# Optimization experiments

Measured on AMD Instinct MI355X. Metric: run time of the kernel, lower is better.

Reference implementation:

```python
import jax, jax.numpy as jnp
import numpy as np

N_E, N_R, E = 100000, 1000, 1000000
E_HID, R_HID = 128, 128
NEG_SLOPE = 0.01


def _seg_softmax(logits, seg, num_segments):
    # torch_geometric.utils.softmax: per-segment max-subtracted softmax, +1e-16 in denom
    m = jax.ops.segment_max(logits, seg, num_segments=num_segments)
    m = jnp.where(jnp.isfinite(m), m, 0.0)  # empty segments
    z = jnp.exp(logits - m[seg])
    s = jax.ops.segment_sum(z, seg, num_segments=num_segments)
    return z / (s[seg] + 1e-16)


def setup_inputs() -> dict:
    key = jax.random.key(0)
    ks = jax.random.split(key, 10)
    s_e = 1.0 / np.sqrt(E_HID)
    s_r = 1.0 / np.sqrt(R_HID)
    s_2r = 1.0 / np.sqrt(2 * R_HID)
    return {
        "x_e": jax.random.normal(ks[0], (N_E, E_HID), jnp.float32),
        "x_r": jax.random.normal(ks[1], (N_R, R_HID), jnp.float32),
        "edge_index": jax.random.randint(ks[2], (2, E), 0, N_E, jnp.int32),
        "rel": jax.random.randint(ks[3], (E,), 0, N_R, jnp.int32),
        "rel_all": jax.random.randint(ks[4], (N_R,), 0, N_R, jnp.int32),
        "w_ah": jax.random.uniform(ks[5], (E_HID,), jnp.float32, -s_e, s_e),
        "w_at": jax.random.uniform(ks[6], (E_HID,), jnp.float32, -s_e, s_e),
        "w_ar": jax.random.uniform(ks[7], (R_HID,), jnp.float32, -s_r, s_r),
        "W_r1": jax.random.uniform(ks[8], (R_HID, 2 * R_HID), jnp.float32, -s_r, s_r),
        "b_r1": jnp.zeros((2 * R_HID,), jnp.float32),
        "W_r2": jax.random.uniform(ks[9], (2 * R_HID, R_HID), jnp.float32, -s_2r, s_2r),
        "b_r2": jnp.zeros((R_HID,), jnp.float32),
        "W_r": jax.random.uniform(jax.random.fold_in(key, 99), (2 * R_HID, 2 * R_HID), jnp.float32, -s_2r, s_2r),
        "b_r": jnp.zeros((2 * R_HID,), jnp.float32),
    }


def reference(x_e, x_r, edge_index, rel, rel_all, w_ah, w_at, w_ar,
              W_r1, b_r1, W_r2, b_r2, W_r, b_r):
    h, t = edge_index[0], edge_index[1]
    n_e = x_e.shape[0]

    # per-node/per-rel attention scores, gathered per edge
    e_h = (x_e @ w_ah)[h]          # [E]
    e_t = (x_e @ w_at)[t]          # [E]
    e_r = (x_r @ w_ar)[rel]        # [E]

    alpha_h = _seg_softmax(jax.nn.leaky_relu(e_h + e_r, NEG_SLOPE), h, n_e)
    alpha_t = _seg_softmax(jax.nn.leaky_relu(e_t + e_r, NEG_SLOPE), t, n_e)

    # relation transform (no activation in original)
    x_r2 = (x_r @ W_r1 + b_r1) @ W_r2 + b_r2   # [N_r, r_hidden]
    msg = x_r + x_r2                            # [N_r, r_hidden]

    # sparse.mm(adj, msg) == weighted scatter-add over edges
    msg_e = msg[rel]                            # [E, r_hidden]
    x_e_h = jax.ops.segment_sum(alpha_h[:, None] * msg_e, h, num_segments=n_e)
    x_e_t = jax.ops.segment_sum(alpha_t[:, None] * msg_e, t, num_segments=n_e)

    x = jnp.concatenate([x_e_h, x_e_t], axis=1)  # [N_e, 2*r_hidden]
    return x @ W_r + b_r
```

## Files before the change

### kernel.cpp

```cpp
#include <hip/hip_runtime.h>
#include <hip/hip_fp16.h>


#define CH1    2048
#define SUPW   4096
#define CAP1   45056
#define CH2    4096
#define CHUNK2 (CAP1 / CH2)
#define NBPS   128
#define CAP2   512
#define MAXD   64

#define MIX_LO(acc, w, z) \
    asm("v_fma_mix_f32 %0, %1, %2, %0 op_sel:[0,0,0] op_sel_hi:[1,0,0]" \
        : "+v"(acc) : "v"(w), "v"(z))
#define MIX_HI(acc, w, z) \
    asm("v_fma_mix_f32 %0, %1, %2, %0 op_sel:[1,0,0] op_sel_hi:[1,0,0]" \
        : "+v"(acc) : "v"(w), "v"(z))

__global__ __launch_bounds__(256) void k_scores(
    const float* __restrict__ xe, const float* __restrict__ xr,
    const float* __restrict__ wah, const float* __restrict__ wat, const float* __restrict__ war,
    float* __restrict__ eh, float* __restrict__ et, float* __restrict__ er,
    int nE, int nR) {
    int wid = (blockIdx.x * blockDim.x + threadIdx.x) >> 6;
    int lane = threadIdx.x & 63;
    if (wid < nE) {
        float2 x2 = *(const float2*)(xe + (size_t)wid * 128 + lane * 2);
        float2 a2 = *(const float2*)(wah + lane * 2);
        float2 b2 = *(const float2*)(wat + lane * 2);
        float dh = x2.x * a2.x + x2.y * a2.y;
        float dt = x2.x * b2.x + x2.y * b2.y;
        #pragma unroll
        for (int m = 32; m >= 1; m >>= 1) { dh += __shfl_xor(dh, m); dt += __shfl_xor(dt, m); }
        if (lane == 0) { eh[wid] = dh; et[wid] = dt; }
    } else if (wid < nE + nR) {
        int r = wid - nE;
        float2 x2 = *(const float2*)(xr + (size_t)r * 128 + lane * 2);
        float2 c2 = *(const float2*)(war + lane * 2);
        float d = x2.x * c2.x + x2.y * c2.y;
        #pragma unroll
        for (int m = 32; m >= 1; m >>= 1) d += __shfl_xor(d, m);
        if (lane == 0) er[r] = d;
    }
}

__global__ __launch_bounds__(256) void k_rel(
    const float* __restrict__ xr,
    const float* __restrict__ W1, const float* __restrict__ b1,
    const float* __restrict__ W2, const float* __restrict__ b2,
    const float* __restrict__ Wr,
    __half* __restrict__ Mh, __half* __restrict__ Mt) {
    __shared__ float xs[128];
    __shared__ float hs[256];
    __shared__ float ms[128];
    int r = blockIdx.x, j = threadIdx.x;
    if (j < 128) xs[j] = xr[(size_t)r * 128 + j];
    __syncthreads();
    {
        float acc = b1[j];
        #pragma unroll 4
        for (int k = 0; k < 128; ++k) acc += xs[k] * W1[k * 256 + j];
        hs[j] = acc;
    }
    __syncthreads();
    if (j < 128) {
        float acc = b2[j] + xs[j];
        #pragma unroll 4
        for (int k = 0; k < 256; ++k) acc += hs[k] * W2[k * 128 + j];
        ms[j] = acc;
    }
    __syncthreads();
    {
        float ah = 0.f, at_ = 0.f;
        #pragma unroll 4
        for (int i = 0; i < 128; ++i) {
            float m = ms[i];
            ah  += m * Wr[i * 256 + j];
            at_ += m * Wr[(128 + i) * 256 + j];
        }
        Mh[(size_t)r * 256 + j] = __float2half(ah);
        Mt[(size_t)r * 256 + j] = __float2half(at_);
    }
}

__global__ __launch_bounds__(256) void k_hist1(
    const int* __restrict__ ei, int* __restrict__ hist, int E) {
    __shared__ int cnt[64];
    int tid = threadIdx.x;
    if (tid < 64) cnt[tid] = 0;
    __syncthreads();
    int base = blockIdx.x * CH1;
    #pragma unroll
    for (int k = 0; k < CH1 / 256; ++k) {
        int e = base + k * 256 + tid;
        if (e < E) {
            unsigned vh = ((unsigned)ei[e]) << 1;
            unsigned vt = (((unsigned)ei[E + e]) << 1) | 1u;
            atomicAdd(&cnt[vh >> 12], 1);
            atomicAdd(&cnt[vt >> 12], 1);
        }
    }
    __syncthreads();
    if (tid < 64) hist[tid * 512 + blockIdx.x] = cnt[tid];
}

__global__ __launch_bounds__(256) void k_scanp(
    int* __restrict__ hist, int* __restrict__ bcur1,
    int* __restrict__ bcur2, int nbuck, int nblk) {
    __shared__ int wtot[4];
    int bin = blockIdx.x, tid = threadIdx.x, lane = tid & 63, wid = tid >> 6;
    for (int g = bin * 256 + tid; g < nbuck; g += 64 * 256) bcur2[g] = 0;
    int j0 = 2 * tid, j1 = 2 * tid + 1;
    int v0 = (j0 < nblk) ? hist[bin * 512 + j0] : 0;
    int v1 = (j1 < nblk) ? hist[bin * 512 + j1] : 0;
    int ts = v0 + v1;
    int incl = ts;
    #pragma unroll
    for (int d = 1; d < 64; d <<= 1) { int u = __shfl_up(incl, d); if (lane >= d) incl += u; }
    if (lane == 63) wtot[wid] = incl;
    __syncthreads();
    int wbase = 0;
    for (int w = 0; w < wid; ++w) wbase += wtot[w];
    int excl = wbase + incl - ts;
    hist[bin * 512 + j0] = excl;
    hist[bin * 512 + j1] = excl + v0;
    if (tid == 255) bcur1[bin] = wbase + incl;
}

__global__ __launch_bounds__(256) void k_part1(
    const int* __restrict__ ei, const int* __restrict__ rel,
    const int* __restrict__ hist, unsigned* __restrict__ part1, int E) {
    __shared__ unsigned stage[CH1 * 2];
    __shared__ int cnt[64], offs_[64], cur[64], gb[64];
    int tid = threadIdx.x;
    if (tid < 64) cnt[tid] = 0;
    __syncthreads();
    int base = blockIdx.x * CH1;
    unsigned wh[CH1 / 256], wt[CH1 / 256];
    bool ve[CH1 / 256];
    #pragma unroll
    for (int k = 0; k < CH1 / 256; ++k) {
        int e = base + k * 256 + tid;
        ve[k] = (e < E);
        unsigned h = 0, t = 0, r = 0;
        if (ve[k]) { h = (unsigned)ei[e]; t = (unsigned)ei[E + e]; r = (unsigned)rel[e]; }
        unsigned vh = h << 1, vt = (t << 1) | 1u;
        wh[k] = ((vh >> 12) << 26) | ((vh & 4095u) << 10) | r;
        wt[k] = ((vt >> 12) << 26) | ((vt & 4095u) << 10) | r;
        if (ve[k]) { atomicAdd(&cnt[wh[k] >> 26], 1); atomicAdd(&cnt[wt[k] >> 26], 1); }
    }
    __syncthreads();
    if (tid < 64) {
        int v = cnt[tid], incl = v;
        #pragma unroll
        for (int d = 1; d < 64; d <<= 1) { int u = __shfl_up(incl, d); if (tid >= d) incl += u; }
        offs_[tid] = incl - v;
        cur[tid] = incl - v;
        gb[tid] = hist[tid * 512 + blockIdx.x];
    }
    __syncthreads();
    #pragma unroll
    for (int k = 0; k < CH1 / 256; ++k) {
        if (ve[k]) {
            int p = atomicAdd(&cur[wh[k] >> 26], 1); stage[p] = wh[k];
            int q = atomicAdd(&cur[wt[k] >> 26], 1); stage[q] = wt[k];
        }
    }
    __syncthreads();
    int total = offs_[63] + cnt[63];
    for (int p = tid; p < total; p += 256) {
        unsigned w = stage[p];
        int bin = w >> 26;
        int dst = gb[bin] + (p - offs_[bin]);
        if (dst < CAP1) part1[(size_t)bin * CAP1 + dst] = w & 0x03FFFFFFu;
    }
}

__global__ __launch_bounds__(256) void k_part2(
    const int* __restrict__ bcur1, const unsigned* __restrict__ part1,
    int* __restrict__ bcur2, unsigned short* __restrict__ part2) {
    int s = blockIdx.x / CHUNK2, c = blockIdx.x % CHUNK2;
    int cnt_s = min(bcur1[s], CAP1);
    int start = c * CH2;
    if (start >= cnt_s) return;
    __shared__ unsigned stage[CH2];
    __shared__ int cnt[NBPS], offs_[NBPS], cur[NBPS], gb[NBPS];
    __shared__ int wt2[2];
    int tid = threadIdx.x;
    if (tid < NBPS) cnt[tid] = 0;
    __syncthreads();
    unsigned w_[CH2 / 256];
    bool v_[CH2 / 256];
    #pragma unroll
    for (int k = 0; k < CH2 / 256; ++k) {
        int i = start + k * 256 + tid;
        v_[k] = (i < cnt_s);
        unsigned it = v_[k] ? part1[(size_t)s * CAP1 + i] : 0u;
        unsigned sb = ((it >> 10) & 4095u) >> 5;
        unsigned entry = (((it >> 10) & 31u) << 10) | (it & 1023u);
        w_[k] = (sb << 16) | entry;
        if (v_[k]) atomicAdd(&cnt[sb], 1);
    }
    __syncthreads();
    int v128 = 0, incl128 = 0;
    if (tid < NBPS) {
        v128 = cnt[tid]; incl128 = v128;
        int lane = tid & 63;
        #pragma unroll
        for (int d = 1; d < 64; d <<= 1) { int u = __shfl_up(incl128, d); if (lane >= d) incl128 += u; }
        if (lane == 63) wt2[tid >> 6] = incl128;
    }
    __syncthreads();
    if (tid < NBPS) {
        int base2 = (tid >= 64) ? wt2[0] : 0;
        int excl = base2 + incl128 - v128;
        offs_[tid] = excl;
        cur[tid] = excl;
        gb[tid] = atomicAdd(&bcur2[s * NBPS + tid], v128);
    }
    __syncthreads();
    #pragma unroll
    for (int k = 0; k < CH2 / 256; ++k)
        if (v_[k]) { int p = atomicAdd(&cur[w_[k] >> 16], 1); stage[p] = w_[k]; }
    __syncthreads();
    int total = offs_[NBPS - 1] + cnt[NBPS - 1];
    for (int p = tid; p < total; p += 256) {
        unsigned w = stage[p];
        int sb = w >> 16;
        int dst = gb[sb] + (p - offs_[sb]);
        if (dst < CAP2) part2[((size_t)s * NBPS + sb) * CAP2 + dst] = (unsigned short)w;
    }
}

__global__ __launch_bounds__(256) void k_group_out9(
    const int* __restrict__ bcur2, const unsigned short* __restrict__ part2,
    const float* __restrict__ eh, const float* __restrict__ et, const float* __restrict__ er,
    const __half* __restrict__ Mh, const __half* __restrict__ Mt,
    const float* __restrict__ br, float* __restrict__ out, int nE, int nR) {
    __shared__ unsigned short csr[CAP2];
    __shared__ float er_s[1024];
    __shared__ unsigned zbuf[4][2][64];
    __shared__ int cnt[32], offs_[32], cur[32];
    int b = blockIdx.x, tid = threadIdx.x;
    int count = min(bcur2[b], CAP2);
    if (tid < 32) cnt[tid] = 0;
    for (int i = tid; i < nR; i += 256) er_s[i] = er[i];
    __syncthreads();
    unsigned short ev[CAP2 / 256];
    bool val[CAP2 / 256];
    #pragma unroll
    for (int k = 0; k < CAP2 / 256; ++k) {
        int i = tid + k * 256;
        val[k] = (i < count);
        ev[k] = val[k] ? part2[(size_t)b * CAP2 + i] : (unsigned short)0;
        if (val[k]) atomicAdd(&cnt[ev[k] >> 10], 1);
    }
    __syncthreads();
    if (tid < 32) {
        int v = cnt[tid], incl = v;
        #pragma unroll
        for (int d = 1; d < 32; d <<= 1) { int u = __shfl_up(incl, d); if (tid >= d) incl += u; }
        offs_[tid] = incl - v;
        cur[tid] = incl - v;
    }
    __syncthreads();
    #pragma unroll
    for (int k = 0; k < CAP2 / 256; ++k) {
        if (val[k]) {
            int p = atomicAdd(&cur[ev[k] >> 10], 1);
            csr[p] = (unsigned short)(ev[k] & 1023u);
        }
    }
    __syncthreads();
    int lane = tid & 63, wid = tid >> 6;
    int half = lane >> 5, l31 = lane & 31;
    const __half* MB = (half ? Mt : Mh) + (l31 << 3);
    float4 bv = *(const float4*)(br + l31 * 8 + half * 4);
    int nbase = b * 16;
    for (int li = wid; li < 16; li += 4) {
        int n = nbase + li;
        if (n >= nE) break;
        int oH = offs_[2 * li];
        int oT = offs_[2 * li + 1];
        int dH = min(cur[2 * li] - oH, MAXD);
        int dT = min(cur[2 * li + 1] - oT, MAXD);
        float ehn = eh[n], etn = et[n];
        unsigned eHv = 0u, eTv = 0u;
        if (lane < dH) {
            int r = csr[oH + lane];
            float l = ehn + er_s[r]; l = l > 0.f ? l : 0.01f * l;
            eHv = (__float_as_uint(__expf(l)) & 0xFFFFFC00u) | (unsigned)r;
        }
        if (lane < dT) {
            int r = csr[oT + lane];
            float l = etn + er_s[r]; l = l > 0.f ? l : 0.01f * l;
            eTv = (__float_as_uint(__expf(l)) & 0xFFFFFC00u) | (unsigned)r;
        }
        zbuf[wid][0][lane] = eHv;
        zbuf[wid][1][lane] = eTv;
        const unsigned* zrow = &zbuf[wid][half][0];
        float acc[8] = {0, 0, 0, 0, 0, 0, 0, 0};
        float s = 0.f;
        int kk = (max(dH, dT) + 3) & ~3;
        for (int j = 0; j < kk; j += 4) {
            uint4 cc = *(const uint4*)(zrow + j);
            unsigned carr[4] = {cc.x, cc.y, cc.z, cc.w};
            #pragma unroll
            for (int i = 0; i < 4; ++i) {
                unsigned c = carr[i];
                float z = __uint_as_float(c & 0xFFFFFC00u);
                uint4 m = *(const uint4*)(MB + (((size_t)(c & 0x3FFu)) << 8));
                MIX_LO(acc[0], m.x, z); MIX_HI(acc[1], m.x, z);
                MIX_LO(acc[2], m.y, z); MIX_HI(acc[3], m.y, z);
                MIX_LO(acc[4], m.z, z); MIX_HI(acc[5], m.z, z);
                MIX_LO(acc[6], m.w, z); MIX_HI(acc[7], m.w, z);
                s += z;
            }
        }
        float sO = __shfl_xor(s, 32);
        float iMine = 1.f / (s + 1e-16f);
        float iOther = 1.f / (sO + 1e-16f);
        float4 o;
        float oq[4];
        #pragma unroll
        for (int q = 0; q < 4; ++q) {
            float send = half ? acc[q] : acc[4 + q];
            float mine = half ? acc[4 + q] : acc[q];
            float recv = __shfl_xor(send, 32);
            oq[q] = mine * iMine + recv * iOther;
        }
        o.x = oq[0] + bv.x;
        o.y = oq[1] + bv.y;
        o.z = oq[2] + bv.z;
        o.w = oq[3] + bv.w;
        *(float4*)(out + (size_t)n * 256 + l31 * 8 + half * 4) = o;
    }
}

__global__ __launch_bounds__(256) void k_hist(
    const int* __restrict__ ei, int* __restrict__ deg, int E, int nE) {
    int e = blockIdx.x * blockDim.x + threadIdx.x;
    if (e >= E) return;
    atomicAdd(&deg[ei[e]], 1);
    atomicAdd(&deg[nE + ei[E + e]], 1);
}

__global__ __launch_bounds__(256) void k_scan1(
    const int* __restrict__ deg, int* __restrict__ offs, int* __restrict__ bsum, int N) {
    __shared__ int wtot[4];
    int tid = threadIdx.x, lane = tid & 63, wid = tid >> 6;
    int base = blockIdx.x * 1024 + tid * 4;
    int v[4];
    #pragma unroll
    for (int i = 0; i < 4; ++i) v[i] = (base + i < N) ? deg[base + i] : 0;
    int ts = v[0] + v[1] + v[2] + v[3];
    int incl = ts;
    #pragma unroll
    for (int d = 1; d < 64; d <<= 1) { int u = __shfl_up(incl, d); if (lane >= d) incl += u; }
    if (lane == 63) wtot[wid] = incl;
    __syncthreads();
    int wbase = 0;
    for (int w = 0; w < wid; ++w) wbase += wtot[w];
    int run = wbase + incl - ts;
    #pragma unroll
    for (int i = 0; i < 4; ++i) { if (base + i < N) offs[base + i] = run; run += v[i]; }
    if (tid == 255) bsum[blockIdx.x] = wbase + incl;
}

__global__ __launch_bounds__(256) void k_scan2(int* __restrict__ bsum, int NB) {
    __shared__ int wtot[4];
    int tid = threadIdx.x, lane = tid & 63, wid = tid >> 6;
    int v = (tid < NB) ? bsum[tid] : 0;
    int incl = v;
    #pragma unroll
    for (int d = 1; d < 64; d <<= 1) { int u = __shfl_up(incl, d); if (lane >= d) incl += u; }
    if (lane == 63) wtot[wid] = incl;
    __syncthreads();
    int wbase = 0;
    for (int w = 0; w < wid; ++w) wbase += wtot[w];
    if (tid < NB) bsum[tid] = wbase + incl - v;
}

__global__ __launch_bounds__(256) void k_scan3(
    int* __restrict__ offs, const int* __restrict__ bsum, int* __restrict__ cursor, int N) {
    int i = blockIdx.x * blockDim.x + threadIdx.x;
    if (i >= N) return;
    int v = offs[i] + bsum[i >> 10];
    offs[i] = v;
    cursor[i] = v;
}

__global__ __launch_bounds__(256) void k_scatter_offs(
    const int* __restrict__ ei, const int* __restrict__ rel,
    const float* __restrict__ eh, const float* __restrict__ et, const float* __restrict__ er,
    int* __restrict__ cursor, unsigned* __restrict__ csr, int E, int nE) {
    int e = blockIdx.x * blockDim.x + threadIdx.x;
    if (e >= E) return;
    int h = ei[e], t = ei[E + e], r = rel[e];
    float erv = er[r];
    float lh = eh[h] + erv; lh = lh > 0.f ? lh : 0.01f * lh;
    float lt = et[t] + erv; lt = lt > 0.f ? lt : 0.01f * lt;
    unsigned zh = (__float_as_uint(__expf(lh)) & 0xFFFFFC00u) | (unsigned)r;
    unsigned zt = (__float_as_uint(__expf(lt)) & 0xFFFFFC00u) | (unsigned)r;
    int ph = atomicAdd(&cursor[h], 1);
    csr[ph] = zh;
    int pt = atomicAdd(&cursor[nE + t], 1);
    csr[pt] = zt;
}

__global__ __launch_bounds__(256) void k_out_offs(
    const int* __restrict__ offs, const int* __restrict__ deg, const unsigned* __restrict__ csr,
    const __half* __restrict__ Mh, const __half* __restrict__ Mt, const float* __restrict__ br,
    float* __restrict__ out, int nE) {
    int wid = (blockIdx.x * blockDim.x + threadIdx.x) >> 6;
    int lane = threadIdx.x & 63;
    if (wid >= nE) return;
    int dH = deg[wid], dT = deg[nE + wid];
    size_t offH = (size_t)offs[wid], offT = (size_t)offs[nE + wid];
    float4 accH = {0, 0, 0, 0}, accT = {0, 0, 0, 0};
    float sH = 0.f, sT = 0.f;
    int dM = max(dH, dT);
    for (int b = 0; b < dM; b += 64) {
        int kH = min(64, dH - b);
        int kT = min(64, dT - b);
        unsigned eH = 0, eT = 0;
        if (lane < kH) eH = csr[offH + b + lane];
        if (lane < kT) eT = csr[offT + b + lane];
        int kk = max(kH, kT);
        for (int j = 0; j < kk; ++j) {
            unsigned cH = (unsigned)__shfl((int)eH, j);
            unsigned cT = (unsigned)__shfl((int)eT, j);
            if (j < kH) {
                float z = __uint_as_float(cH & 0xFFFFFC00u);
                int r = (int)(cH & 0x3FFu);
                const __half2* mp = (const __half2*)(Mh + ((size_t)r << 8) + (lane << 2));
                float2 m01 = __half22float2(mp[0]);
                float2 m23 = __half22float2(mp[1]);
                accH.x += z * m01.x; accH.y += z * m01.y;
                accH.z += z * m23.x; accH.w += z * m23.y;
                sH += z;
            }
            if (j < kT) {
                float z = __uint_as_float(cT & 0xFFFFFC00u);
                int r = (int)(cT & 0x3FFu);
                const __half2* mp = (const __half2*)(Mt + ((size_t)r << 8) + (lane << 2));
                float2 m01 = __half22float2(mp[0]);
                float2 m23 = __half22float2(mp[1]);
                accT.x += z * m01.x; accT.y += z * m01.y;
                accT.z += z * m23.x; accT.w += z * m23.y;
                sT += z;
            }
        }
    }
    float iH = 1.f / (sH + 1e-16f);
    float iT = 1.f / (sT + 1e-16f);
    float4 bv = *(const float4*)(br + lane * 4);
    float4 o;
    o.x = accH.x * iH + accT.x * iT + bv.x;
    o.y = accH.y * iH + accT.y * iT + bv.y;
    o.z = accH.z * iH + accT.z * iT + bv.z;
    o.w = accH.w * iH + accT.w * iT + bv.w;
    *(float4*)(out + (size_t)wid * 256 + lane * 4) = o;
}

extern "C" void kernel_launch(void* const* d_in, const int* in_sizes, int n_in,
                              void* d_out, int out_size, void* d_ws, size_t ws_size,
                              hipStream_t stream) {
    const float* xe  = (const float*)d_in[0];
    const float* xr  = (const float*)d_in[1];
    const int*   ei  = (const int*)d_in[2];
    const int*   rel = (const int*)d_in[3];
    const float* wah = (const float*)d_in[5];
    const float* wat = (const float*)d_in[6];
    const float* war = (const float*)d_in[7];
    const float* W1  = (const float*)d_in[8];
    const float* b1  = (const float*)d_in[9];
    const float* W2  = (const float*)d_in[10];
    const float* b2  = (const float*)d_in[11];
    const float* Wr  = (const float*)d_in[12];
    const float* br  = (const float*)d_in[13];
    float* out = (float*)d_out;

    const int nE = in_sizes[0] / 128;
    const int nR = in_sizes[1] / 128;
    const int E  = in_sizes[3];
    const int N  = 2 * nE;
    const int NSUP  = (N + SUPW - 1) / SUPW;
    const int NBUCK = NSUP * NBPS;
    const int NBLK1 = (E + CH1 - 1) / CH1;

    float* ws = (float*)d_ws;
    size_t o = 0;
    auto alloc = [&](size_t words) { size_t r = o; o += (words + 3) & ~(size_t)3; return r; };
    float* eh     = ws + alloc(nE);
    float* et     = ws + alloc(nE);
    float* er     = ws + alloc(nR);
    __half* Mh    = (__half*)(ws + alloc((size_t)nR * 128));
    __half* Mt    = (__half*)(ws + alloc((size_t)nR * 128));
    size_t common_words = o;

    size_t hist_words  = 64 * 512;
    size_t part1_words = (size_t)NSUP * CAP1;
    size_t part2_words = ((size_t)NBUCK * CAP2 + 1) / 2;
    size_t new_words = hist_words + 64 + NBUCK + part1_words + part2_words;
    bool planNew = (NBLK1 <= 512) && (NSUP <= 64) &&
                   (ws_size >= (common_words + new_words + 64) * 4);

    k_scores<<<(nE + nR + 3) / 4, 256, 0, stream>>>(xe, xr, wah, wat, war, eh, et, er, nE, nR);
    k_rel<<<nR, 256, 0, stream>>>(xr, W1, b1, W2, b2, Wr, Mh, Mt);

    if (planNew) {
        int* hist   = (int*)(ws + alloc(hist_words));
        int* bcur1  = (int*)(ws + alloc(64));
        int* bcur2  = (int*)(ws + alloc(NBUCK));
        unsigned* part1 = (unsigned*)(ws + alloc(part1_words));
        unsigned short* part2 = (unsigned short*)(ws + alloc(part2_words));
        k_hist1<<<NBLK1, 256, 0, stream>>>(ei, hist, E);
        k_scanp<<<64, 256, 0, stream>>>(hist, bcur1, bcur2, NBUCK, NBLK1);
        k_part1<<<NBLK1, 256, 0, stream>>>(ei, rel, hist, part1, E);
        k_part2<<<NSUP * CHUNK2, 256, 0, stream>>>(bcur1, part1, bcur2, part2);
        k_group_out9<<<NBUCK, 256, 0, stream>>>(bcur2, part2, eh, et, er, Mh, Mt, br, out, nE, nR);
    } else {
        int* cursor = (int*)(ws + alloc(N));
        int* deg    = (int*)(ws + alloc(N));
        int* offs   = (int*)(ws + alloc(N));
        int* bsum   = (int*)(ws + alloc(512));
        unsigned* csr = (unsigned*)(ws + alloc(2 * (size_t)E));
        const int NB = (N + 1023) / 1024;
        hipMemsetAsync(deg, 0, (size_t)N * sizeof(int), stream);
        k_hist<<<(E + 255) / 256, 256, 0, stream>>>(ei, deg, E, nE);
        k_scan1<<<NB, 256, 0, stream>>>(deg, offs, bsum, N);
        k_scan2<<<1, 256, 0, stream>>>(bsum, NB);
        k_scan3<<<(N + 255) / 256, 256, 0, stream>>>(offs, bsum, cursor, N);
        k_scatter_offs<<<(E + 255) / 256, 256, 0, stream>>>(ei, rel, eh, et, er, cursor, csr, E, nE);
        k_out_offs<<<(nE + 3) / 4, 256, 0, stream>>>(offs, deg, csr, Mh, Mt, br, out, nE);
    }
}
```

Measured before the change: 314.9 us.

## Fuse score, relation-transform and histogram kernels into one front launch

Merges k_scores, k_rel and k_hist1 into a single k_front kernel whose blocks are split by index into three roles. This removes two kernel launches and lets the independent work run concurrently on the GPU. The final group kernel also stores precomputed byte offsets into Mh/Mt in a separate shared buffer, so the inner loop no longer has to unpack and select the pointer. The cost is a heavier kernel with a larger shared-memory footprint, and the three roles now share one launch configuration.

```diff
diff --git a/kernel.cpp b/kernel.cpp
--- a/kernel.cpp
+++ b/kernel.cpp
@@ -17,6 +17,333 @@
 #define MIX_HI(acc, w, z) \
     asm("v_fma_mix_f32 %0, %1, %2, %0 op_sel:[1,0,0] op_sel_hi:[1,0,0]" \
         : "+v"(acc) : "v"(w), "v"(z))
+
+__global__ __launch_bounds__(256) void k_front(
+    const float* __restrict__ xe, const float* __restrict__ xr,
+    const float* __restrict__ wah, const float* __restrict__ wat, const float* __restrict__ war,
+    const float* __restrict__ W1, const float* __restrict__ b1,
+    const float* __restrict__ W2, const float* __restrict__ b2,
+    const float* __restrict__ Wr,
+    const int* __restrict__ ei,
+    float* __restrict__ eh, float* __restrict__ et, float* __restrict__ er,
+    __half* __restrict__ Mh, __half* __restrict__ Mt,
+    int* __restrict__ hist,
+    int nE, int nR, int E, int nSc) {
+    __shared__ float xs[128];
+    __shared__ float hs[256];
+    __shared__ float ms[128];
+    __shared__ int cnt[64];
+    int b = blockIdx.x, tid = threadIdx.x;
+    if (b < nSc) {
+        int wid = b * 4 + (tid >> 6);
+        int lane = tid & 63;
+        if (wid < nE) {
+            float2 x2 = *(const float2*)(xe + (size_t)wid * 128 + lane * 2);
+            float2 a2 = *(const float2*)(wah + lane * 2);
+            float2 b2_ = *(const float2*)(wat + lane * 2);
+            float dh = x2.x * a2.x + x2.y * a2.y;
+            float dt = x2.x * b2_.x + x2.y * b2_.y;
+            #pragma unroll
+            for (int m = 32; m >= 1; m >>= 1) { dh += __shfl_xor(dh, m); dt += __shfl_xor(dt, m); }
+            if (lane == 0) { eh[wid] = dh; et[wid] = dt; }
+        } else if (wid < nE + nR) {
+            int r = wid - nE;
+            float2 x2 = *(const float2*)(xr + (size_t)r * 128 + lane * 2);
+            float2 c2 = *(const float2*)(war + lane * 2);
+            float d = x2.x * c2.x + x2.y * c2.y;
+            #pragma unroll
+            for (int m = 32; m >= 1; m >>= 1) d += __shfl_xor(d, m);
+            if (lane == 0) er[r] = d;
+        }
+    } else if (b < nSc + nR) {
+        int r = b - nSc, j = tid;
+        if (j < 128) xs[j] = xr[(size_t)r * 128 + j];
+        __syncthreads();
+        {
+            float acc = b1[j];
+            #pragma unroll 4
+            for (int k = 0; k < 128; ++k) acc += xs[k] * W1[k * 256 + j];
+            hs[j] = acc;
+        }
+        __syncthreads();
+        if (j < 128) {
+            float acc = b2[j] + xs[j];
+            #pragma unroll 4
+            for (int k = 0; k < 256; ++k) acc += hs[k] * W2[k * 128 + j];
+            ms[j] = acc;
+        }
+        __syncthreads();
+        {
+            float ah = 0.f, at_ = 0.f;
+            #pragma unroll 4
+            for (int i = 0; i < 128; ++i) {
+                float m = ms[i];
+                ah  += m * Wr[i * 256 + j];
+                at_ += m * Wr[(128 + i) * 256 + j];
+            }
+            Mh[(size_t)r * 256 + j] = __float2half(ah);
+            Mt[(size_t)r * 256 + j] = __float2half(at_);
+        }
+    } else {
+        int blk = b - nSc - nR;
+        if (tid < 64) cnt[tid] = 0;
+        __syncthreads();
+        int base = blk * CH1;
+        #pragma unroll
+        for (int k = 0; k < CH1 / 256; ++k) {
+            int e = base + k * 256 + tid;
+            if (e < E) {
+                unsigned vh = ((unsigned)ei[e]) << 1;
+                unsigned vt = (((unsigned)ei[E + e]) << 1) | 1u;
+                atomicAdd(&cnt[vh >> 12], 1);
+                atomicAdd(&cnt[vt >> 12], 1);
+            }
+        }
+        __syncthreads();
+        if (tid < 64) hist[tid * 512 + blk] = cnt[tid];
+    }
+}
+
+__global__ __launch_bounds__(256) void k_scanp(
+    int* __restrict__ hist, int* __restrict__ bcur1,
+    int* __restrict__ bcur2, int nbuck, int nblk) {
+    __shared__ int wtot[4];
+    int bin = blockIdx.x, tid = threadIdx.x, lane = tid & 63, wid = tid >> 6;
+    for (int g = bin * 256 + tid; g < nbuck; g += 64 * 256) bcur2[g] = 0;
+    int j0 = 2 * tid, j1 = 2 * tid + 1;
+    int v0 = (j0 < nblk) ? hist[bin * 512 + j0] : 0;
+    int v1 = (j1 < nblk) ? hist[bin * 512 + j1] : 0;
+    int ts = v0 + v1;
+    int incl = ts;
+    #pragma unroll
+    for (int d = 1; d < 64; d <<= 1) { int u = __shfl_up(incl, d); if (lane >= d) incl += u; }
+    if (lane == 63) wtot[wid] = incl;
+    __syncthreads();
+    int wbase = 0;
+    for (int w = 0; w < wid; ++w) wbase += wtot[w];
+    int excl = wbase + incl - ts;
+    hist[bin * 512 + j0] = excl;
+    hist[bin * 512 + j1] = excl + v0;
+    if (tid == 255) bcur1[bin] = wbase + incl;
+}
+
+__global__ __launch_bounds__(256) void k_part1(
+    const int* __restrict__ ei, const int* __restrict__ rel,
+    const int* __restrict__ hist, unsigned* __restrict__ part1, int E) {
+    __shared__ unsigned stage[CH1 * 2];
+    __shared__ int cnt[64], offs_[64], cur[64], gb[64];
+    int tid = threadIdx.x;
+    if (tid < 64) cnt[tid] = 0;
+    __syncthreads();
+    int base = blockIdx.x * CH1;
+    unsigned wh[CH1 / 256], wt[CH1 / 256];
+    bool ve[CH1 / 256];
+    #pragma unroll
+    for (int k = 0; k < CH1 / 256; ++k) {
+        int e = base + k * 256 + tid;
+        ve[k] = (e < E);
+        unsigned h = 0, t = 0, r = 0;
+        if (ve[k]) { h = (unsigned)ei[e]; t = (unsigned)ei[E + e]; r = (unsigned)rel[e]; }
+        unsigned vh = h << 1, vt = (t << 1) | 1u;
+        wh[k] = ((vh >> 12) << 26) | ((vh & 4095u) << 10) | r;
+        wt[k] = ((vt >> 12) << 26) | ((vt & 4095u) << 10) | r;
+        if (ve[k]) { atomicAdd(&cnt[wh[k] >> 26], 1); atomicAdd(&cnt[wt[k] >> 26], 1); }
+    }
+    __syncthreads();
+    if (tid < 64) {
+        int v = cnt[tid], incl = v;
+        #pragma unroll
+        for (int d = 1; d < 64; d <<= 1) { int u = __shfl_up(incl, d); if (tid >= d) incl += u; }
+        offs_[tid] = incl - v;
+        cur[tid] = incl - v;
+        gb[tid] = hist[tid * 512 + blockIdx.x];
+    }
+    __syncthreads();
+    #pragma unroll
+    for (int k = 0; k < CH1 / 256; ++k) {
+        if (ve[k]) {
+            int p = atomicAdd(&cur[wh[k] >> 26], 1); stage[p] = wh[k];
+            int q = atomicAdd(&cur[wt[k] >> 26], 1); stage[q] = wt[k];
+        }
+    }
+    __syncthreads();
+    int total = offs_[63] + cnt[63];
+    for (int p = tid; p < total; p += 256) {
+        unsigned w = stage[p];
+        int bin = w >> 26;
+        int dst = gb[bin] + (p - offs_[bin]);
+        if (dst < CAP1) part1[(size_t)bin * CAP1 + dst] = w & 0x03FFFFFFu;
+    }
+}
+
+__global__ __launch_bounds__(256) void k_part2(
+    const int* __restrict__ bcur1, const unsigned* __restrict__ part1,
+    int* __restrict__ bcur2, unsigned short* __restrict__ part2) {
+    int s = blockIdx.x / CHUNK2, c = blockIdx.x % CHUNK2;
+    int cnt_s = min(bcur1[s], CAP1);
+    int start = c * CH2;
+    if (start >= cnt_s) return;
+    __shared__ unsigned stage[CH2];
+    __shared__ int cnt[NBPS], offs_[NBPS], cur[NBPS], gb[NBPS];
+    __shared__ int wt2[2];
+    int tid = threadIdx.x;
+    if (tid < NBPS) cnt[tid] = 0;
+    __syncthreads();
+    unsigned w_[CH2 / 256];
+    bool v_[CH2 / 256];
+    #pragma unroll
+    for (int k = 0; k < CH2 / 256; ++k) {
+        int i = start + k * 256 + tid;
+        v_[k] = (i < cnt_s);
+        unsigned it = v_[k] ? part1[(size_t)s * CAP1 + i] : 0u;
+        unsigned sb = ((it >> 10) & 4095u) >> 5;
+        unsigned entry = (((it >> 10) & 31u) << 10) | (it & 1023u);
+        w_[k] = (sb << 16) | entry;
+        if (v_[k]) atomicAdd(&cnt[sb], 1);
+    }
+    __syncthreads();
+    int v128 = 0, incl128 = 0;
+    if (tid < NBPS) {
+        v128 = cnt[tid]; incl128 = v128;
+        int lane = tid & 63;
+        #pragma unroll
+        for (int d = 1; d < 64; d <<= 1) { int u = __shfl_up(incl128, d); if (lane >= d) incl128 += u; }
+        if (lane == 63) wt2[tid >> 6] = incl128;
+    }
+    __syncthreads();
+    if (tid < NBPS) {
+        int base2 = (tid >= 64) ? wt2[0] : 0;
+        int excl = base2 + incl128 - v128;
+        offs_[tid] = excl;
+        cur[tid] = excl;
+        gb[tid] = atomicAdd(&bcur2[s * NBPS + tid], v128);
+    }
+    __syncthreads();
+    #pragma unroll
+    for (int k = 0; k < CH2 / 256; ++k)
+        if (v_[k]) { int p = atomicAdd(&cur[w_[k] >> 16], 1); stage[p] = w_[k]; }
+    __syncthreads();
+    int total = offs_[NBPS - 1] + cnt[NBPS - 1];
+    for (int p = tid; p < total; p += 256) {
+        unsigned w = stage[p];
+        int sb = w >> 16;
+        int dst = gb[sb] + (p - offs_[sb]);
+        if (dst < CAP2) part2[((size_t)s * NBPS + sb) * CAP2 + dst] = (unsigned short)w;
+    }
+}
+
+__global__ __launch_bounds__(256) void k_group_out10(
+    const int* __restrict__ bcur2, const unsigned short* __restrict__ part2,
+    const float* __restrict__ eh, const float* __restrict__ et, const float* __restrict__ er,
+    const __half* __restrict__ Mh, const __half* __restrict__ Mt,
+    const float* __restrict__ br, float* __restrict__ out, int nE, int nR) {
+    __shared__ unsigned short csr[CAP2];
+    __shared__ float er_s[1024];
+    __shared__ unsigned zbufZ[4][2][64];
+    __shared__ unsigned zbufO[4][2][64];
+    __shared__ int cnt[32], offs_[32], cur[32];
+    int b = blockIdx.x, tid = threadIdx.x;
+    int count = min(bcur2[b], CAP2);
+    unsigned mtOff = (unsigned)nR * 512u;
+    if (tid < 32) cnt[tid] = 0;
+    for (int i = tid; i < nR; i += 256) er_s[i] = er[i];
+    __syncthreads();
+    unsigned short ev[CAP2 / 256];
+    bool val[CAP2 / 256];
+    #pragma unroll
+    for (int k = 0; k < CAP2 / 256; ++k) {
+        int i = tid + k * 256;
+        val[k] = (i < count);
+        ev[k] = val[k] ? part2[(size_t)b * CAP2 + i] : (unsigned short)0;
+        if (val[k]) atomicAdd(&cnt[ev[k] >> 10], 1);
+    }
+    __syncthreads();
+    if (tid < 32) {
+        int v = cnt[tid], incl = v;
+        #pragma unroll
+        for (int d = 1; d < 32; d <<= 1) { int u = __shfl_up(incl, d); if (tid >= d) incl += u; }
+        offs_[tid] = incl - v;
+        cur[tid] = incl - v;
+    }
+    __syncthreads();
+    #pragma unroll
+    for (int k = 0; k < CAP2 / 256; ++k) {
+        if (val[k]) {
+            int p = atomicAdd(&cur[ev[k] >> 10], 1);
+            csr[p] = (unsigned short)(ev[k] & 1023u);
+        }
+    }
+    __syncthreads();
+    int lane = tid & 63, wid = tid >> 6;
+    int half = lane >> 5, l31 = lane & 31;
+    unsigned loff = (unsigned)(l31 << 4);
+    const char* Mbase = (const char*)Mh;
+    float4 bv = *(const float4*)(br + l31 * 8 + half * 4);
+    int nbase = b * 16;
+    for (int li = wid; li < 16; li += 4) {
+        int n = nbase + li;
+        if (n >= nE) break;
+        int oH = offs_[2 * li];
+        int oT = offs_[2 * li + 1];
+        int dH = min(cur[2 * li] - oH, MAXD);
+        int dT = min(cur[2 * li + 1] - oT, MAXD);
+        float ehn = eh[n], etn = et[n];
+        unsigned zHv = 0u, oHv = 0u;
+        unsigned zTv = 0u, oTv = mtOff;
+        if (lane < dH) {
+            int r = csr[oH + lane];
+            float l = ehn + er_s[r]; l = l > 0.f ? l : 0.01f * l;
+            zHv = __float_as_uint(__expf(l)) & 0xFFFFFC00u;
+            oHv = (unsigned)r << 9;
+        }
+        if (lane < dT) {
+            int r = csr[oT + lane];
+            float l = etn + er_s[r]; l = l > 0.f ? l : 0.01f * l;
+            zTv = __float_as_uint(__expf(l)) & 0xFFFFFC00u;
+            oTv = ((unsigned)r << 9) + mtOff;
+        }
+        zbufZ[wid][0][lane] = zHv; zbufO[wid][0][lane] = oHv;
+        zbufZ[wid][1][lane] = zTv; zbufO[wid][1][lane] = oTv;
+        const unsigned* zrowZ = &zbufZ[wid][half][0];
+        const unsigned* zrowO = &zbufO[wid][half][0];
+        float acc[8] = {0, 0, 0, 0, 0, 0, 0, 0};
+        float s = 0.f;
+        int kk = (max(dH, dT) + 3) & ~3;
+        for (int j = 0; j < kk; j += 4) {
+            uint4 z4 = *(const uint4*)(zrowZ + j);
+            uint4 o4 = *(const uint4*)(zrowO + j);
+            unsigned za[4] = {z4.x, z4.y, z4.z, z4.w};
+            unsigned oa[4] = {o4.x, o4.y, o4.z, o4.w};
+            #pragma unroll
+            for (int i = 0; i < 4; ++i) {
+                float z = __uint_as_float(za[i]);
+                uint4 m = *(const uint4*)(Mbase + (oa[i] + loff));
+                MIX_LO(acc[0], m.x, z); MIX_HI(acc[1], m.x, z);
+                MIX_LO(acc[2], m.y, z); MIX_HI(acc[3], m.y, z);
+                MIX_LO(acc[4], m.z, z); MIX_HI(acc[5], m.z, z);
+                MIX_LO(acc[6], m.w, z); MIX_HI(acc[7], m.w, z);
+                s += z;
+            }
+        }
+        float sO = __shfl_xor(s, 32);
+        float iMine = 1.f / (s + 1e-16f);
+        float iOther = 1.f / (sO + 1e-16f);
+        float oq[4];
+        #pragma unroll
+        for (int q = 0; q < 4; ++q) {
+            float send = half ? acc[q] : acc[4 + q];
+            float mine = half ? acc[4 + q] : acc[q];
+            float recv = __shfl_xor(send, 32);
+            oq[q] = mine * iMine + recv * iOther;
+        }
+        float4 o;
+        o.x = oq[0] + bv.x;
+        o.y = oq[1] + bv.y;
+        o.z = oq[2] + bv.z;
+        o.w = oq[3] + bv.w;
+        *(float4*)(out + (size_t)n * 256 + l31 * 8 + half * 4) = o;
+    }
+}
 
 __global__ __launch_bounds__(256) void k_scores(
     const float* __restrict__ xe, const float* __restrict__ xr,
@@ -81,260 +408,6 @@
         }
         Mh[(size_t)r * 256 + j] = __float2half(ah);
         Mt[(size_t)r * 256 + j] = __float2half(at_);
-    }
-}
-
-__global__ __launch_bounds__(256) void k_hist1(
-    const int* __restrict__ ei, int* __restrict__ hist, int E) {
-    __shared__ int cnt[64];
-    int tid = threadIdx.x;
-    if (tid < 64) cnt[tid] = 0;
-    __syncthreads();
-    int base = blockIdx.x * CH1;
-    #pragma unroll
-    for (int k = 0; k < CH1 / 256; ++k) {
-        int e = base + k * 256 + tid;
-        if (e < E) {
-            unsigned vh = ((unsigned)ei[e]) << 1;
-            unsigned vt = (((unsigned)ei[E + e]) << 1) | 1u;
-            atomicAdd(&cnt[vh >> 12], 1);
-            atomicAdd(&cnt[vt >> 12], 1);
-        }
-    }
-    __syncthreads();
-    if (tid < 64) hist[tid * 512 + blockIdx.x] = cnt[tid];
-}
-
-__global__ __launch_bounds__(256) void k_scanp(
-    int* __restrict__ hist, int* __restrict__ bcur1,
-    int* __restrict__ bcur2, int nbuck, int nblk) {
-    __shared__ int wtot[4];
-    int bin = blockIdx.x, tid = threadIdx.x, lane = tid & 63, wid = tid >> 6;
-    for (int g = bin * 256 + tid; g < nbuck; g += 64 * 256) bcur2[g] = 0;
-    int j0 = 2 * tid, j1 = 2 * tid + 1;
-    int v0 = (j0 < nblk) ? hist[bin * 512 + j0] : 0;
-    int v1 = (j1 < nblk) ? hist[bin * 512 + j1] : 0;
-    int ts = v0 + v1;
-    int incl = ts;
-    #pragma unroll
-    for (int d = 1; d < 64; d <<= 1) { int u = __shfl_up(incl, d); if (lane >= d) incl += u; }
-    if (lane == 63) wtot[wid] = incl;
-    __syncthreads();
-    int wbase = 0;
-    for (int w = 0; w < wid; ++w) wbase += wtot[w];
-    int excl = wbase + incl - ts;
-    hist[bin * 512 + j0] = excl;
-    hist[bin * 512 + j1] = excl + v0;
-    if (tid == 255) bcur1[bin] = wbase + incl;
-}
-
-__global__ __launch_bounds__(256) void k_part1(
-    const int* __restrict__ ei, const int* __restrict__ rel,
-    const int* __restrict__ hist, unsigned* __restrict__ part1, int E) {
-    __shared__ unsigned stage[CH1 * 2];
-    __shared__ int cnt[64], offs_[64], cur[64], gb[64];
-    int tid = threadIdx.x;
-    if (tid < 64) cnt[tid] = 0;
-    __syncthreads();
-    int base = blockIdx.x * CH1;
-    unsigned wh[CH1 / 256], wt[CH1 / 256];
-    bool ve[CH1 / 256];
-    #pragma unroll
-    for (int k = 0; k < CH1 / 256; ++k) {
-        int e = base + k * 256 + tid;
-        ve[k] = (e < E);
-        unsigned h = 0, t = 0, r = 0;
-        if (ve[k]) { h = (unsigned)ei[e]; t = (unsigned)ei[E + e]; r = (unsigned)rel[e]; }
-        unsigned vh = h << 1, vt = (t << 1) | 1u;
-        wh[k] = ((vh >> 12) << 26) | ((vh & 4095u) << 10) | r;
-        wt[k] = ((vt >> 12) << 26) | ((vt & 4095u) << 10) | r;
-        if (ve[k]) { atomicAdd(&cnt[wh[k] >> 26], 1); atomicAdd(&cnt[wt[k] >> 26], 1); }
-    }
-    __syncthreads();
-    if (tid < 64) {
-        int v = cnt[tid], incl = v;
-        #pragma unroll
-        for (int d = 1; d < 64; d <<= 1) { int u = __shfl_up(incl, d); if (tid >= d) incl += u; }
-        offs_[tid] = incl - v;
-        cur[tid] = incl - v;
-        gb[tid] = hist[tid * 512 + blockIdx.x];
-    }
-    __syncthreads();
-    #pragma unroll
-    for (int k = 0; k < CH1 / 256; ++k) {
-        if (ve[k]) {
-            int p = atomicAdd(&cur[wh[k] >> 26], 1); stage[p] = wh[k];
-            int q = atomicAdd(&cur[wt[k] >> 26], 1); stage[q] = wt[k];
-        }
-    }
-    __syncthreads();
-    int total = offs_[63] + cnt[63];
-    for (int p = tid; p < total; p += 256) {
-        unsigned w = stage[p];
-        int bin = w >> 26;
-        int dst = gb[bin] + (p - offs_[bin]);
-        if (dst < CAP1) part1[(size_t)bin * CAP1 + dst] = w & 0x03FFFFFFu;
-    }
-}
-
-__global__ __launch_bounds__(256) void k_part2(
-    const int* __restrict__ bcur1, const unsigned* __restrict__ part1,
-    int* __restrict__ bcur2, unsigned short* __restrict__ part2) {
-    int s = blockIdx.x / CHUNK2, c = blockIdx.x % CHUNK2;
-    int cnt_s = min(bcur1[s], CAP1);
-    int start = c * CH2;
-    if (start >= cnt_s) return;
-    __shared__ unsigned stage[CH2];
-    __shared__ int cnt[NBPS], offs_[NBPS], cur[NBPS], gb[NBPS];
-    __shared__ int wt2[2];
-    int tid = threadIdx.x;
-    if (tid < NBPS) cnt[tid] = 0;
-    __syncthreads();
-    unsigned w_[CH2 / 256];
-    bool v_[CH2 / 256];
-    #pragma unroll
-    for (int k = 0; k < CH2 / 256; ++k) {
-        int i = start + k * 256 + tid;
-        v_[k] = (i < cnt_s);
-        unsigned it = v_[k] ? part1[(size_t)s * CAP1 + i] : 0u;
-        unsigned sb = ((it >> 10) & 4095u) >> 5;
-        unsigned entry = (((it >> 10) & 31u) << 10) | (it & 1023u);
-        w_[k] = (sb << 16) | entry;
-        if (v_[k]) atomicAdd(&cnt[sb], 1);
-    }
-    __syncthreads();
-    int v128 = 0, incl128 = 0;
-    if (tid < NBPS) {
-        v128 = cnt[tid]; incl128 = v128;
-        int lane = tid & 63;
-        #pragma unroll
-        for (int d = 1; d < 64; d <<= 1) { int u = __shfl_up(incl128, d); if (lane >= d) incl128 += u; }
-        if (lane == 63) wt2[tid >> 6] = incl128;
-    }
-    __syncthreads();
-    if (tid < NBPS) {
-        int base2 = (tid >= 64) ? wt2[0] : 0;
-        int excl = base2 + incl128 - v128;
-        offs_[tid] = excl;
-        cur[tid] = excl;
-        gb[tid] = atomicAdd(&bcur2[s * NBPS + tid], v128);
-    }
-    __syncthreads();
-    #pragma unroll
-    for (int k = 0; k < CH2 / 256; ++k)
-        if (v_[k]) { int p = atomicAdd(&cur[w_[k] >> 16], 1); stage[p] = w_[k]; }
-    __syncthreads();
-    int total = offs_[NBPS - 1] + cnt[NBPS - 1];
-    for (int p = tid; p < total; p += 256) {
-        unsigned w = stage[p];
-        int sb = w >> 16;
-        int dst = gb[sb] + (p - offs_[sb]);
-        if (dst < CAP2) part2[((size_t)s * NBPS + sb) * CAP2 + dst] = (unsigned short)w;
-    }
-}
-
-__global__ __launch_bounds__(256) void k_group_out9(
-    const int* __restrict__ bcur2, const unsigned short* __restrict__ part2,
-    const float* __restrict__ eh, const float* __restrict__ et, const float* __restrict__ er,
-    const __half* __restrict__ Mh, const __half* __restrict__ Mt,
-    const float* __restrict__ br, float* __restrict__ out, int nE, int nR) {
-    __shared__ unsigned short csr[CAP2];
-    __shared__ float er_s[1024];
-    __shared__ unsigned zbuf[4][2][64];
-    __shared__ int cnt[32], offs_[32], cur[32];
-    int b = blockIdx.x, tid = threadIdx.x;
-    int count = min(bcur2[b], CAP2);
-    if (tid < 32) cnt[tid] = 0;
-    for (int i = tid; i < nR; i += 256) er_s[i] = er[i];
-    __syncthreads();
-    unsigned short ev[CAP2 / 256];
-    bool val[CAP2 / 256];
-    #pragma unroll
-    for (int k = 0; k < CAP2 / 256; ++k) {
-        int i = tid + k * 256;
-        val[k] = (i < count);
-        ev[k] = val[k] ? part2[(size_t)b * CAP2 + i] : (unsigned short)0;
-        if (val[k]) atomicAdd(&cnt[ev[k] >> 10], 1);
-    }
-    __syncthreads();
-    if (tid < 32) {
-        int v = cnt[tid], incl = v;
-        #pragma unroll
-        for (int d = 1; d < 32; d <<= 1) { int u = __shfl_up(incl, d); if (tid >= d) incl += u; }
-        offs_[tid] = incl - v;
-        cur[tid] = incl - v;
-    }
-    __syncthreads();
-    #pragma unroll
-    for (int k = 0; k < CAP2 / 256; ++k) {
-        if (val[k]) {
-            int p = atomicAdd(&cur[ev[k] >> 10], 1);
-            csr[p] = (unsigned short)(ev[k] & 1023u);
-        }
-    }
-    __syncthreads();
-    int lane = tid & 63, wid = tid >> 6;
-    int half = lane >> 5, l31 = lane & 31;
-    const __half* MB = (half ? Mt : Mh) + (l31 << 3);
-    float4 bv = *(const float4*)(br + l31 * 8 + half * 4);
-    int nbase = b * 16;
-    for (int li = wid; li < 16; li += 4) {
-        int n = nbase + li;
-        if (n >= nE) break;
-        int oH = offs_[2 * li];
-        int oT = offs_[2 * li + 1];
-        int dH = min(cur[2 * li] - oH, MAXD);
-        int dT = min(cur[2 * li + 1] - oT, MAXD);
-        float ehn = eh[n], etn = et[n];
-        unsigned eHv = 0u, eTv = 0u;
-        if (lane < dH) {
-            int r = csr[oH + lane];
-            float l = ehn + er_s[r]; l = l > 0.f ? l : 0.01f * l;
-            eHv = (__float_as_uint(__expf(l)) & 0xFFFFFC00u) | (unsigned)r;
-        }
-        if (lane < dT) {
-            int r = csr[oT + lane];
-            float l = etn + er_s[r]; l = l > 0.f ? l : 0.01f * l;
-            eTv = (__float_as_uint(__expf(l)) & 0xFFFFFC00u) | (unsigned)r;
-        }
-        zbuf[wid][0][lane] = eHv;
-        zbuf[wid][1][lane] = eTv;
-        const unsigned* zrow = &zbuf[wid][half][0];
-        float acc[8] = {0, 0, 0, 0, 0, 0, 0, 0};
-        float s = 0.f;
-        int kk = (max(dH, dT) + 3) & ~3;
-        for (int j = 0; j < kk; j += 4) {
-            uint4 cc = *(const uint4*)(zrow + j);
-            unsigned carr[4] = {cc.x, cc.y, cc.z, cc.w};
-            #pragma unroll
-            for (int i = 0; i < 4; ++i) {
-                unsigned c = carr[i];
-                float z = __uint_as_float(c & 0xFFFFFC00u);
-                uint4 m = *(const uint4*)(MB + (((size_t)(c & 0x3FFu)) << 8));
-                MIX_LO(acc[0], m.x, z); MIX_HI(acc[1], m.x, z);
-                MIX_LO(acc[2], m.y, z); MIX_HI(acc[3], m.y, z);
-                MIX_LO(acc[4], m.z, z); MIX_HI(acc[5], m.z, z);
-                MIX_LO(acc[6], m.w, z); MIX_HI(acc[7], m.w, z);
-                s += z;
-            }
-        }
-        float sO = __shfl_xor(s, 32);
-        float iMine = 1.f / (s + 1e-16f);
-        float iOther = 1.f / (sO + 1e-16f);
-        float4 o;
-        float oq[4];
-        #pragma unroll
-        for (int q = 0; q < 4; ++q) {
-            float send = half ? acc[q] : acc[4 + q];
-            float mine = half ? acc[4 + q] : acc[q];
-            float recv = __shfl_xor(send, 32);
-            oq[q] = mine * iMine + recv * iOther;
-        }
-        o.x = oq[0] + bv.x;
-        o.y = oq[1] + bv.y;
-        o.z = oq[2] + bv.z;
-        o.w = oq[3] + bv.w;
-        *(float4*)(out + (size_t)n * 256 + l31 * 8 + half * 4) = o;
     }
 }
 
@@ -489,6 +562,7 @@
     const int NSUP  = (N + SUPW - 1) / SUPW;
     const int NBUCK = NSUP * NBPS;
     const int NBLK1 = (E + CH1 - 1) / CH1;
+    const int NSC   = (nE + nR + 3) / 4;
 
     float* ws = (float*)d_ws;
     size_t o = 0;
@@ -507,20 +581,19 @@
     bool planNew = (NBLK1 <= 512) && (NSUP <= 64) &&
                    (ws_size >= (common_words + new_words + 64) * 4);
 
-    k_scores<<<(nE + nR + 3) / 4, 256, 0, stream>>>(xe, xr, wah, wat, war, eh, et, er, nE, nR);
-    k_rel<<<nR, 256, 0, stream>>>(xr, W1, b1, W2, b2, Wr, Mh, Mt);
-
     if (planNew) {
         int* hist   = (int*)(ws + alloc(hist_words));
         int* bcur1  = (int*)(ws + alloc(64));
         int* bcur2  = (int*)(ws + alloc(NBUCK));
         unsigned* part1 = (unsigned*)(ws + alloc(part1_words));
         unsigned short* part2 = (unsigned short*)(ws + alloc(part2_words));
-        k_hist1<<<NBLK1, 256, 0, stream>>>(ei, hist, E);
+        k_front<<<NSC + nR + NBLK1, 256, 0, stream>>>(
+            xe, xr, wah, wat, war, W1, b1, W2, b2, Wr, ei,
+            eh, et, er, Mh, Mt, hist, nE, nR, E, NSC);
         k_scanp<<<64, 256, 0, stream>>>(hist, bcur1, bcur2, NBUCK, NBLK1);
         k_part1<<<NBLK1, 256, 0, stream>>>(ei, rel, hist, part1, E);
         k_part2<<<NSUP * CHUNK2, 256, 0, stream>>>(bcur1, part1, bcur2, part2);
-        k_group_out9<<<NBUCK, 256, 0, stream>>>(bcur2, part2, eh, et, er, Mh, Mt, br, out, nE, nR);
+        k_group_out10<<<NBUCK, 256, 0, stream>>>(bcur2, part2, eh, et, er, Mh, Mt, br, out, nE, nR);
     } else {
         int* cursor = (int*)(ws + alloc(N));
         int* deg    = (int*)(ws + alloc(N));
@@ -528,6 +601,8 @@
         int* bsum   = (int*)(ws + alloc(512));
         unsigned* csr = (unsigned*)(ws + alloc(2 * (size_t)E));
         const int NB = (N + 1023) / 1024;
+        k_scores<<<(nE + nR + 3) / 4, 256, 0, stream>>>(xe, xr, wah, wat, war, eh, et, er, nE, nR);
+        k_rel<<<nR, 256, 0, stream>>>(xr, W1, b1, W2, b2, Wr, Mh, Mt);
         hipMemsetAsync(deg, 0, (size_t)N * sizeof(int), stream);
         k_hist<<<(E + 255) / 256, 256, 0, stream>>>(ei, deg, E, nE);
         k_scan1<<<NB, 256, 0, stream>>>(deg, offs, bsum, N);
```

After: 304.2 us. -3.4%, faster.
